# Kernel optimization log

Hardware: AMD Instinct MI355X
Metric: run time of the kernel (lower is better)

## Reference

```python
import jax, jax.numpy as jnp
import numpy as np
import math

B_GRAPHS = 256
L_NODES = 64
N_NODES = B_GRAPHS * L_NODES
N_EDGES = N_NODES * 4
HEADS = 8
D_INNER = 512
N_DAGS = 1
DIAMETER = 64


def setup_inputs() -> dict:
    key = jax.random.key(0)
    ks = jax.random.split(key, 8)
    x = jax.random.normal(ks[0], (N_NODES, D_INNER), jnp.float32)
    B = jax.random.normal(ks[1], (N_NODES, D_INNER), jnp.float32)
    C = jax.random.normal(ks[2], (N_NODES, D_INNER), jnp.float32)
    dt = jax.random.normal(ks[3], (N_NODES, N_DAGS * HEADS * 2), jnp.float32)
    dt_edge = jax.random.normal(ks[4], (N_EDGES, N_DAGS * HEADS), jnp.float32)
    # DAG edges: within each graph, src_local < dst_local (gap 1..7) -> strictly upper triangular
    u = jax.random.randint(ks[5], (N_EDGES,), 0, L_NODES - 1)
    gap = jax.random.randint(ks[6], (N_EDGES,), 1, 8)
    v = jnp.minimum(u + gap, L_NODES - 1)
    graph = jnp.arange(N_EDGES) // (N_EDGES // B_GRAPHS)
    edge_index = jnp.stack([graph * L_NODES + u, graph * L_NODES + v]).astype(jnp.int32)
    data_batch = (jnp.arange(N_NODES) // L_NODES).astype(jnp.int32)
    dag_masks = jnp.ones((N_DAGS, N_EDGES), jnp.float32)
    # dt_bias init as in module __init__ (inverse softplus of dt in [1e-3, 1e-1])
    rng = np.random.default_rng(0)
    dtv = np.exp(rng.uniform(size=(HEADS,)) * (math.log(0.1) - math.log(0.001)) + math.log(0.001))
    dtv = np.clip(dtv, 1e-4, None)
    dt_bias = jnp.asarray(dtv + np.log(-np.expm1(-dtv)), jnp.float32)
    D = jnp.ones((HEADS,), jnp.float32)
    return dict(x=x, B=B, C=C, dt=dt, dt_edge=dt_edge, dt_bias=dt_bias, D=D,
                dag_masks=dag_masks, edge_index=edge_index, data_batch=data_batch,
                diameter=DIAMETER)


def _repeated_squaring_inverse(A, diam):
    # (I - A)^{-1} = prod_k (I + A^{2^k}) for nilpotent A; O(log diam) matmuls
    j = 2 ** int(math.ceil(math.log2(diam)))
    I = jnp.eye(A.shape[-1], dtype=A.dtype)
    last = A
    M = I + A
    for _ in range(2, int(math.log2(j)) + 1):
        last = last @ last
        M = M @ (I + last)
    return M


def reference(x, B, C, dt, dt_edge, dt_bias, D, dag_masks, edge_index, data_batch, diameter):
    N, din = x.shape
    g, E = dag_masks.shape
    n = dt_bias.shape[0]
    b = int(data_batch[-1]) + 1
    l = N // b  # equal-size graphs -> dense batching is a reshape, mask all-True
    h = din // n
    src, dst = edge_index[0], edge_index[1]

    # dt_node: (N, g*n*c) -> (c, g, n, N); softplus(dt + bias)
    c = dt.shape[1] // (g * n)
    dtn = dt.reshape(N, g, n, c).transpose(3, 1, 2, 0)
    dtn = jax.nn.softplus(dtn + dt_bias[None, None, :, None])
    dte = dt_edge.reshape(E, g, n).transpose(1, 2, 0)  # (g,n,E)
    dte = jax.nn.softplus(dte + dt_bias[None, :, None])

    dt_s, dt_t = dtn[0], dtn[1]
    dt_sum = (dt_s[:, :, src] + dt_t[:, :, dst] + dte) / np.sqrt(3.0)  # (g,n,E)
    dt_exp = jnp.exp(-dt_sum)
    msk = dag_masks[:, None, :]
    dt_sum = dt_sum * msk
    dt_exp = dt_exp * msk

    # dense adjacency with per-edge attrs; note 'b l1 l2 (g n) -> b g n l2 l1' transpose
    b_e = src // l
    sl = src % l
    dl = dst % l
    attr = dt_exp.transpose(2, 0, 1).reshape(E, g * n)
    adj = jnp.zeros((b, l, l, g * n), x.dtype).at[b_e, sl, dl].add(attr)
    A = adj.reshape(b, l, l, g, n).transpose(0, 3, 4, 2, 1)  # (b,g,n,l,l)

    # normalize_mat: sqrt outer product of in-degree counts, clamped at 1
    ec = jnp.zeros((g, N), x.dtype).at[:, dst].add(dag_masks)
    ec_dense = ec.T.reshape(b, l, g)
    outer = jnp.sqrt(jnp.einsum('blg,btg->bglt', ec_dense, ec_dense))
    outer = jnp.where(outer < 1.0, 1.0, outer)
    A = A / outer[:, :, None]

    dnorm = jnp.zeros((g, n, N), x.dtype).at[:, :, dst].add(dt_sum)
    dnorm = dnorm.transpose(2, 0, 1).reshape(b, l, g, n).transpose(0, 2, 3, 1)  # (b,g,n,l)

    A2 = A.reshape(b, g * n, l, l).astype(jnp.float32)
    L = _repeated_squaring_inverse(A2, int(diameter))
    L = L.reshape(b, g, n, l, l) * dnorm[..., None]

    x4 = x.reshape(b, l, n, h).transpose(0, 2, 1, 3)  # (b,n,l,h)
    B3 = B.reshape(b, l, -1)
    C3 = C.reshape(b, l, -1)
    # y = einsum(C,L,B,x) with B/C broadcast over (g,n): fold C.B^T into L
    CB = jnp.einsum('bld,btd->blt', C3, B3)
    M = L * CB[:, None, None]
    y = jnp.einsum('bgnlt,bnth->bgnlh', M, x4)
    y = y + x4[:, None] * D[None, None, :, None, None]
    y = y.transpose(0, 3, 1, 2, 4).reshape(N, g, n * h)  # b g n l h -> (N, g, n*h)
    y = y.sum(axis=1) / np.sqrt(g)
    return y
```

## Files before the change

kernel.cpp:

```cpp
#include <hip/hip_runtime.h>
#include <math.h>

#define NGRAPH 256
#define HEADS  8
#define DIN    512
#define EPG    256
#define NEDGE  65536
#define LOG2E 1.44269504088896341f
#define LN2   0.69314718055994531f

typedef short bf16x8 __attribute__((ext_vector_type(8)));
typedef float f32x4 __attribute__((ext_vector_type(4)));

__device__ __forceinline__ float softplusf(float v) {
    if (v > 20.f) return v;
    float t = exp2f(v * LOG2E);
    return LN2 * log2f(1.f + t);
}
__device__ __forceinline__ unsigned short f2bf(float f) {
    union { float f; unsigned u; } c; c.f = f;
    unsigned r = c.u + 0x7fffu + ((c.u >> 16) & 1u);
    return (unsigned short)(r >> 16);
}
__device__ __forceinline__ float bf2f(unsigned short h) {
    union { float f; unsigned u; } c; c.u = ((unsigned)h) << 16;
    return c.f;
}
__device__ __forceinline__ int swz_idx(int row, int t) {
    int g = ((t >> 3) ^ (row ^ (row >> 3))) & 7;
    return (row << 6) | (g << 3) | (t & 7);
}
__device__ __forceinline__ void split1(float f, unsigned short& hi, unsigned short& lo) {
    union { float f; unsigned q; } c; c.f = f;
    unsigned hb = c.q & 0xffff0000u;
    hi = (unsigned short)(hb >> 16);
    union { float f; unsigned q; } d; d.q = hb;
    union { float f; unsigned q; } e2; e2.f = f - d.f;
    lo = (unsigned short)(e2.q >> 16);
}

__device__ __forceinline__ void stage_chunk(int c, unsigned short* buf,
                                            const float* __restrict__ Cm,
                                            const float* __restrict__ Bm,
                                            int b, int tid) {
    #pragma unroll
    for (int i = 0; i < 4; ++i) {
        int u = tid * 4 + i;
        int mat = u >> 10;
        int rem = u & 1023;
        int row = rem >> 4;
        int col4 = (rem & 15) << 2;
        const float* src = (mat ? Bm : Cm) + ((size_t)(b * 64 + row)) * DIN + c * 64 + col4;
        float4 v = *(const float4*)src;
        float a[4] = {v.x, v.y, v.z, v.w};
        unsigned long long hp = 0, lp = 0;
        #pragma unroll
        for (int k = 0; k < 4; ++k) {
            unsigned short h, l;
            split1(a[k], h, l);
            hp |= ((unsigned long long)h) << (16 * k);
            lp |= ((unsigned long long)l) << (16 * k);
        }
        int idx = swz_idx(row, col4);
        unsigned short* thi = buf + (mat ? 8192 : 0);
        *(unsigned long long*)(thi + idx) = hp;
        *(unsigned long long*)(thi + 4096 + idx) = lp;
    }
}

__global__ __launch_bounds__(512, 2) void dag_fused_v3(
        const float* __restrict__ x,
        const float* __restrict__ Bm,
        const float* __restrict__ Cm,
        const float* __restrict__ dt,
        const float* __restrict__ dt_edge,
        const float* __restrict__ dt_bias,
        const float* __restrict__ Dp,
        const float* __restrict__ dag_masks,
        const int* __restrict__ edge_index,
        float* __restrict__ out) {
    __shared__ __align__(16) unsigned short WS[32768];
    __shared__ __align__(16) unsigned short Xt[HEADS][4096];
    __shared__ __align__(16) unsigned short CBsh[4096];
    __shared__ float Ab[HEADS][448];
    __shared__ float dts[HEADS][64];
    __shared__ float dtt[HEADS][64];
    __shared__ float dnsh[HEADS][64];
    __shared__ float ecsh[64];

    const int b = blockIdx.x;
    const int tid = threadIdx.x;
    const int w = tid >> 6;
    const int lane = tid & 63;
    const int lm = lane & 15;
    const int quad = lane >> 4;
    const float bias = dt_bias[w];

    {
        float2 dv = *(const float2*)(dt + ((size_t)(b * 64 + lane)) * 16 + w * 2);
        dts[w][lane] = softplusf(dv.x + bias);
        dtt[w][lane] = softplusf(dv.y + bias);
        dnsh[w][lane] = 0.f;
        #pragma unroll
        for (int s = 0; s < 7; ++s) Ab[w][lane * 7 + s] = 0.f;
        if (w == 0) ecsh[lane] = 0.f;
    }

    {
        #pragma unroll
        for (int eo = 0; eo < 4; ++eo) {
            int e = b * EPG + eo * 64 + lane;
            int sl = edge_index[e] & 63;
            int dl = edge_index[NEDGE + e] & 63;
            float mk = dag_masks[e];
            float de = softplusf(dt_edge[(size_t)e * HEADS + w] + bias);
            float dsum = (dts[w][sl] + dtt[w][dl] + de) * 0.57735026918962576451f;
            float dexp = exp2f(-dsum * LOG2E);
            atomicAdd(&Ab[w][dl * 7 + (dl - sl - 1)], dexp * mk);
            atomicAdd(&dnsh[w][dl], dsum * mk);
            if (w == 0) atomicAdd(&ecsh[dl], mk);
        }
    }

    {
        const float* xg = x + (size_t)b * 64 * DIN + w * 64;
        #pragma unroll
        for (int r = 0; r < 4; ++r) {
            int t0 = quad * 4 + r * 16;
            int e0 = lm * 4;
            float4 v0 = *(const float4*)(xg + (size_t)(t0 + 0) * DIN + e0);
            float4 v1 = *(const float4*)(xg + (size_t)(t0 + 1) * DIN + e0);
            float4 v2 = *(const float4*)(xg + (size_t)(t0 + 2) * DIN + e0);
            float4 v3 = *(const float4*)(xg + (size_t)(t0 + 3) * DIN + e0);
            float a0[4] = {v0.x, v0.y, v0.z, v0.w};
            float a1[4] = {v1.x, v1.y, v1.z, v1.w};
            float a2[4] = {v2.x, v2.y, v2.z, v2.w};
            float a3[4] = {v3.x, v3.y, v3.z, v3.w};
            #pragma unroll
            for (int k = 0; k < 4; ++k) {
                unsigned long long pk =
                      (unsigned long long)f2bf(a0[k])
                    | ((unsigned long long)f2bf(a1[k]) << 16)
                    | ((unsigned long long)f2bf(a2[k]) << 32)
                    | ((unsigned long long)f2bf(a3[k]) << 48);
                *(unsigned long long*)(&Xt[w][swz_idx(e0 + k, t0)]) = pk;
            }
        }
    }

    const int mi = w >> 1;
    const int ni0 = (w & 1) * 2;
    f32x4 acc0 = {0.f, 0.f, 0.f, 0.f};
    f32x4 acc1 = {0.f, 0.f, 0.f, 0.f};
    stage_chunk(0, WS, Cm, Bm, b, tid);
    for (int c = 0; c < 8; ++c) {
        __syncthreads();
        if (c < 7) stage_chunk(c + 1, WS + ((c + 1) & 1) * 16384, Cm, Bm, b, tid);
        const unsigned short* p = WS + (c & 1) * 16384;
        #pragma unroll
        for (int ks = 0; ks < 2; ++ks) {
            int kl = ks * 32 + quad * 8;
            bf16x8 ah  = *(const bf16x8*)(p +         swz_idx(mi * 16 + lm, kl));
            bf16x8 al  = *(const bf16x8*)(p +  4096 + swz_idx(mi * 16 + lm, kl));
            bf16x8 b0h = *(const bf16x8*)(p +  8192 + swz_idx(ni0 * 16 + lm, kl));
            bf16x8 b0l = *(const bf16x8*)(p + 12288 + swz_idx(ni0 * 16 + lm, kl));
            bf16x8 b1h = *(const bf16x8*)(p +  8192 + swz_idx((ni0 + 1) * 16 + lm, kl));
            bf16x8 b1l = *(const bf16x8*)(p + 12288 + swz_idx((ni0 + 1) * 16 + lm, kl));
            acc0 = __builtin_amdgcn_mfma_f32_16x16x32_bf16(ah, b0h, acc0, 0, 0, 0);
            acc0 = __builtin_amdgcn_mfma_f32_16x16x32_bf16(ah, b0l, acc0, 0, 0, 0);
            acc0 = __builtin_amdgcn_mfma_f32_16x16x32_bf16(al, b0h, acc0, 0, 0, 0);
            acc1 = __builtin_amdgcn_mfma_f32_16x16x32_bf16(ah, b1h, acc1, 0, 0, 0);
            acc1 = __builtin_amdgcn_mfma_f32_16x16x32_bf16(ah, b1l, acc1, 0, 0, 0);
            acc1 = __builtin_amdgcn_mfma_f32_16x16x32_bf16(al, b1h, acc1, 0, 0, 0);
        }
    }
    #pragma unroll
    for (int r = 0; r < 4; ++r) {
        int row = mi * 16 + quad * 4 + r;
        CBsh[row * 64 + ni0 * 16 + lm] = f2bf(acc0[r]);
        CBsh[row * 64 + (ni0 + 1) * 16 + lm] = f2bf(acc1[r]);
    }
    __syncthreads();

    {
        float eci = ecsh[lane];
        #pragma unroll
        for (int s = 0; s < 7; ++s) {
            int src = lane - 1 - s;
            if (src >= 0) {
                float p = eci * ecsh[src];
                float f = fminf(1.f, rsqrtf(p));
                Ab[w][lane * 7 + s] *= f;
            }
        }
    }

    unsigned short* Wlw = WS + w * 4096;
    {
        const int j = lane;
        const float Dh = Dp[w];
        float mwin[7] = {0.f, 0.f, 0.f, 0.f, 0.f, 0.f, 0.f};
        float cab[7];
        #pragma unroll
        for (int s = 0; s < 7; ++s) cab[s] = Ab[w][s];
        float cbv = bf2f(CBsh[j]);
        float dnv = dnsh[w][0];
        for (int i = 0; i < 64; ++i) {
            float nab[7], ncb = 0.f, ndn = 0.f;
            if (i < 63) {
                #pragma unroll
                for (int s = 0; s < 7; ++s) nab[s] = Ab[w][(i + 1) * 7 + s];
                ncb = bf2f(CBsh[(i + 1) * 64 + j]);
                ndn = dnsh[w][i + 1];
            } else {
                #pragma unroll
                for (int s = 0; s < 7; ++s) nab[s] = 0.f;
            }
            float diag = (j == i) ? 1.f : 0.f;
            float t0 = fmaf(cab[0], mwin[0], fmaf(cab[1], mwin[1], diag));
            float t1 = fmaf(cab[2], mwin[2], fmaf(cab[3], mwin[3], cab[4] * mwin[4]));
            float t2 = fmaf(cab[5], mwin[5], cab[6] * mwin[6]);
            float mi_ = t0 + (t1 + t2);
            float wv = mi_ * cbv * dnv;
            if (j == i) wv += Dh;
            Wlw[swz_idx(i, j)] = f2bf(wv);
            #pragma unroll
            for (int s = 6; s > 0; --s) mwin[s] = mwin[s - 1];
            mwin[0] = mi_;
            #pragma unroll
            for (int s = 0; s < 7; ++s) cab[s] = nab[s];
            cbv = ncb;
            dnv = ndn;
        }
    }

    {
        bf16x8 bf[4][2];
        #pragma unroll
        for (int eb = 0; eb < 4; ++eb) {
            int er = eb * 16 + lm;
            bf[eb][0] = *(const bf16x8*)(&Xt[w][swz_idx(er, quad * 8)]);
            bf[eb][1] = *(const bf16x8*)(&Xt[w][swz_idx(er, 32 + quad * 8)]);
        }
        float* og = out + (size_t)b * 64 * DIN + w * 64;
        #pragma unroll
        for (int m2 = 0; m2 < 4; ++m2) {
            int row0 = m2 * 16 + lm;
            bf16x8 a0 = *(const bf16x8*)(&Wlw[swz_idx(row0, quad * 8)]);
            bf16x8 a1 = *(const bf16x8*)(&Wlw[swz_idx(row0, 32 + quad * 8)]);
            f32x4 acc[4];
            #pragma unroll
            for (int eb = 0; eb < 4; ++eb) {
                f32x4 z = {0.f, 0.f, 0.f, 0.f};
                z = __builtin_amdgcn_mfma_f32_16x16x32_bf16(a0, bf[eb][0], z, 0, 0, 0);
                z = __builtin_amdgcn_mfma_f32_16x16x32_bf16(a1, bf[eb][1], z, 0, 0, 0);
                acc[eb] = z;
            }
            #pragma unroll
            for (int r = 0; r < 4; ++r) {
                int row = m2 * 16 + quad * 4 + r;
                #pragma unroll
                for (int eb = 0; eb < 4; ++eb)
                    og[(size_t)row * DIN + eb * 16 + lm] = acc[eb][r];
            }
        }
    }
}

extern "C" void kernel_launch(void* const* d_in, const int* in_sizes, int n_in,
                              void* d_out, int out_size, void* d_ws, size_t ws_size,
                              hipStream_t stream) {
    (void)in_sizes; (void)n_in; (void)out_size; (void)d_ws; (void)ws_size;
    dag_fused_v3<<<dim3(NGRAPH), dim3(512), 0, stream>>>(
        (const float*)d_in[0],
        (const float*)d_in[1],
        (const float*)d_in[2],
        (const float*)d_in[3],
        (const float*)d_in[4],
        (const float*)d_in[5],
        (const float*)d_in[6],
        (const float*)d_in[7],
        (const int*)d_in[8],
        (float*)d_out);
}
```

Measured before the change: 163.6 us.

## Split each graph across two blocks by head halves, redundantly computing C·B^T

```diff
diff --git a/kernel.cpp b/kernel.cpp
--- a/kernel.cpp
+++ b/kernel.cpp
@@ -30,6 +30,10 @@
     int g = ((t >> 3) ^ (row ^ (row >> 3))) & 7;
     return (row << 6) | (g << 3) | (t & 7);
 }
+__device__ __forceinline__ int swz32(int row, int t) {
+    int g = ((t >> 3) ^ (row & 3) ^ ((row >> 2) & 3)) & 3;
+    return row * 32 + g * 8 + (t & 7);
+}
 __device__ __forceinline__ void split1(float f, unsigned short& hi, unsigned short& lo) {
     union { float f; unsigned q; } c; c.f = f;
     unsigned hb = c.q & 0xffff0000u;
@@ -39,18 +43,16 @@
     lo = (unsigned short)(e2.q >> 16);
 }
 
-__device__ __forceinline__ void stage_chunk(int c, unsigned short* buf,
-                                            const float* __restrict__ Cm,
-                                            const float* __restrict__ Bm,
-                                            int b, int tid) {
+__device__ __forceinline__ void stage32(int c, unsigned short* buf,
+                                        const float* __restrict__ Cm,
+                                        const float* __restrict__ Bm,
+                                        int b, int tid) {
     #pragma unroll
     for (int i = 0; i < 4; ++i) {
-        int u = tid * 4 + i;
-        int mat = u >> 10;
-        int rem = u & 1023;
-        int row = rem >> 4;
-        int col4 = (rem & 15) << 2;
-        const float* src = (mat ? Bm : Cm) + ((size_t)(b * 64 + row)) * DIN + c * 64 + col4;
+        int rem = ((i & 1) << 8) + tid;
+        int row = rem >> 3;
+        int col4 = (rem & 7) << 2;
+        const float* src = ((i >> 1) ? Bm : Cm) + ((size_t)(b * 64 + row)) * DIN + c * 32 + col4;
         float4 v = *(const float4*)src;
         float a[4] = {v.x, v.y, v.z, v.w};
         unsigned long long hp = 0, lp = 0;
@@ -61,14 +63,14 @@
             hp |= ((unsigned long long)h) << (16 * k);
             lp |= ((unsigned long long)l) << (16 * k);
         }
-        int idx = swz_idx(row, col4);
-        unsigned short* thi = buf + (mat ? 8192 : 0);
-        *(unsigned long long*)(thi + idx) = hp;
-        *(unsigned long long*)(thi + 4096 + idx) = lp;
-    }
-}
-
-__global__ __launch_bounds__(512, 2) void dag_fused_v3(
+        int idx = swz32(row, col4);
+        unsigned short* t2 = buf + (i >> 1) * 4096;
+        *(unsigned long long*)(t2 + idx) = hp;
+        *(unsigned long long*)(t2 + 2048 + idx) = lp;
+    }
+}
+
+__global__ __launch_bounds__(256, 3) void dag_split_v4(
         const float* __restrict__ x,
         const float* __restrict__ Bm,
         const float* __restrict__ Cm,
@@ -79,31 +81,34 @@
         const float* __restrict__ dag_masks,
         const int* __restrict__ edge_index,
         float* __restrict__ out) {
-    __shared__ __align__(16) unsigned short WS[32768];
-    __shared__ __align__(16) unsigned short Xt[HEADS][4096];
+    __shared__ __align__(16) unsigned short WS[16384];
     __shared__ __align__(16) unsigned short CBsh[4096];
-    __shared__ float Ab[HEADS][448];
-    __shared__ float dts[HEADS][64];
-    __shared__ float dtt[HEADS][64];
-    __shared__ float dnsh[HEADS][64];
-    __shared__ float ecsh[64];
-
-    const int b = blockIdx.x;
+    __shared__ __align__(16) float Ab8[4][512];
+    __shared__ float dts[4][64];
+    __shared__ float dtt[4][64];
+    __shared__ float dnsh[4][64];
+    __shared__ float ecsh[4][64];
+
+    const int gid = blockIdx.x;
+    const int b = gid & 255;
+    const int half = gid >> 8;
     const int tid = threadIdx.x;
     const int w = tid >> 6;
     const int lane = tid & 63;
     const int lm = lane & 15;
     const int quad = lane >> 4;
-    const float bias = dt_bias[w];
-
-    {
-        float2 dv = *(const float2*)(dt + ((size_t)(b * 64 + lane)) * 16 + w * 2);
+    const int h = half * 4 + w;
+    const float bias = dt_bias[h];
+
+    {
+        float2 dv = *(const float2*)(dt + ((size_t)(b * 64 + lane)) * 16 + h * 2);
         dts[w][lane] = softplusf(dv.x + bias);
         dtt[w][lane] = softplusf(dv.y + bias);
         dnsh[w][lane] = 0.f;
-        #pragma unroll
-        for (int s = 0; s < 7; ++s) Ab[w][lane * 7 + s] = 0.f;
-        if (w == 0) ecsh[lane] = 0.f;
+        ecsh[w][lane] = 0.f;
+        float4 z = make_float4(0.f, 0.f, 0.f, 0.f);
+        *(float4*)(&Ab8[w][lane * 8]) = z;
+        *(float4*)(&Ab8[w][lane * 8 + 4]) = z;
     }
 
     {
@@ -113,113 +118,86 @@
             int sl = edge_index[e] & 63;
             int dl = edge_index[NEDGE + e] & 63;
             float mk = dag_masks[e];
-            float de = softplusf(dt_edge[(size_t)e * HEADS + w] + bias);
+            float de = softplusf(dt_edge[(size_t)e * HEADS + h] + bias);
             float dsum = (dts[w][sl] + dtt[w][dl] + de) * 0.57735026918962576451f;
             float dexp = exp2f(-dsum * LOG2E);
-            atomicAdd(&Ab[w][dl * 7 + (dl - sl - 1)], dexp * mk);
+            atomicAdd(&Ab8[w][dl * 8 + (dl - sl)], dexp * mk);
             atomicAdd(&dnsh[w][dl], dsum * mk);
-            if (w == 0) atomicAdd(&ecsh[dl], mk);
-        }
-    }
-
-    {
-        const float* xg = x + (size_t)b * 64 * DIN + w * 64;
-        #pragma unroll
-        for (int r = 0; r < 4; ++r) {
-            int t0 = quad * 4 + r * 16;
-            int e0 = lm * 4;
-            float4 v0 = *(const float4*)(xg + (size_t)(t0 + 0) * DIN + e0);
-            float4 v1 = *(const float4*)(xg + (size_t)(t0 + 1) * DIN + e0);
-            float4 v2 = *(const float4*)(xg + (size_t)(t0 + 2) * DIN + e0);
-            float4 v3 = *(const float4*)(xg + (size_t)(t0 + 3) * DIN + e0);
-            float a0[4] = {v0.x, v0.y, v0.z, v0.w};
-            float a1[4] = {v1.x, v1.y, v1.z, v1.w};
-            float a2[4] = {v2.x, v2.y, v2.z, v2.w};
-            float a3[4] = {v3.x, v3.y, v3.z, v3.w};
-            #pragma unroll
-            for (int k = 0; k < 4; ++k) {
-                unsigned long long pk =
-                      (unsigned long long)f2bf(a0[k])
-                    | ((unsigned long long)f2bf(a1[k]) << 16)
-                    | ((unsigned long long)f2bf(a2[k]) << 32)
-                    | ((unsigned long long)f2bf(a3[k]) << 48);
-                *(unsigned long long*)(&Xt[w][swz_idx(e0 + k, t0)]) = pk;
-            }
-        }
-    }
-
-    const int mi = w >> 1;
-    const int ni0 = (w & 1) * 2;
-    f32x4 acc0 = {0.f, 0.f, 0.f, 0.f};
-    f32x4 acc1 = {0.f, 0.f, 0.f, 0.f};
-    stage_chunk(0, WS, Cm, Bm, b, tid);
-    for (int c = 0; c < 8; ++c) {
-        __syncthreads();
-        if (c < 7) stage_chunk(c + 1, WS + ((c + 1) & 1) * 16384, Cm, Bm, b, tid);
-        const unsigned short* p = WS + (c & 1) * 16384;
-        #pragma unroll
-        for (int ks = 0; ks < 2; ++ks) {
-            int kl = ks * 32 + quad * 8;
-            bf16x8 ah  = *(const bf16x8*)(p +         swz_idx(mi * 16 + lm, kl));
-            bf16x8 al  = *(const bf16x8*)(p +  4096 + swz_idx(mi * 16 + lm, kl));
-            bf16x8 b0h = *(const bf16x8*)(p +  8192 + swz_idx(ni0 * 16 + lm, kl));
-            bf16x8 b0l = *(const bf16x8*)(p + 12288 + swz_idx(ni0 * 16 + lm, kl));
-            bf16x8 b1h = *(const bf16x8*)(p +  8192 + swz_idx((ni0 + 1) * 16 + lm, kl));
-            bf16x8 b1l = *(const bf16x8*)(p + 12288 + swz_idx((ni0 + 1) * 16 + lm, kl));
-            acc0 = __builtin_amdgcn_mfma_f32_16x16x32_bf16(ah, b0h, acc0, 0, 0, 0);
-            acc0 = __builtin_amdgcn_mfma_f32_16x16x32_bf16(ah, b0l, acc0, 0, 0, 0);
-            acc0 = __builtin_amdgcn_mfma_f32_16x16x32_bf16(al, b0h, acc0, 0, 0, 0);
-            acc1 = __builtin_amdgcn_mfma_f32_16x16x32_bf16(ah, b1h, acc1, 0, 0, 0);
-            acc1 = __builtin_amdgcn_mfma_f32_16x16x32_bf16(ah, b1l, acc1, 0, 0, 0);
-            acc1 = __builtin_amdgcn_mfma_f32_16x16x32_bf16(al, b1h, acc1, 0, 0, 0);
-        }
-    }
-    #pragma unroll
-    for (int r = 0; r < 4; ++r) {
-        int row = mi * 16 + quad * 4 + r;
-        CBsh[row * 64 + ni0 * 16 + lm] = f2bf(acc0[r]);
-        CBsh[row * 64 + (ni0 + 1) * 16 + lm] = f2bf(acc1[r]);
-    }
-    __syncthreads();
-
-    {
-        float eci = ecsh[lane];
+            atomicAdd(&ecsh[w][dl], mk);
+        }
+    }
+
+    {
+        float eci = ecsh[w][lane];
+        float4 a03 = *(const float4*)(&Ab8[w][lane * 8]);
+        float4 a47 = *(const float4*)(&Ab8[w][lane * 8 + 4]);
+        float sc[7];
         #pragma unroll
         for (int s = 0; s < 7; ++s) {
             int src = lane - 1 - s;
-            if (src >= 0) {
-                float p = eci * ecsh[src];
-                float f = fminf(1.f, rsqrtf(p));
-                Ab[w][lane * 7 + s] *= f;
-            }
-        }
-    }
+            float p = (src >= 0) ? eci * ecsh[w][src] : 1.f;
+            sc[s] = fminf(1.f, rsqrtf(p));
+        }
+        a03.y *= sc[0]; a03.z *= sc[1]; a03.w *= sc[2];
+        a47.x *= sc[3]; a47.y *= sc[4]; a47.z *= sc[5]; a47.w *= sc[6];
+        *(float4*)(&Ab8[w][lane * 8]) = a03;
+        *(float4*)(&Ab8[w][lane * 8 + 4]) = a47;
+    }
+
+    {
+        f32x4 acc[4];
+        #pragma unroll
+        for (int ni = 0; ni < 4; ++ni) acc[ni] = (f32x4){0.f, 0.f, 0.f, 0.f};
+        stage32(0, WS, Cm, Bm, b, tid);
+        for (int c = 0; c < 16; ++c) {
+            __syncthreads();
+            if (c < 15) stage32(c + 1, WS + ((c + 1) & 1) * 8192, Cm, Bm, b, tid);
+            const unsigned short* p = WS + (c & 1) * 8192;
+            bf16x8 ah = *(const bf16x8*)(p + swz32(w * 16 + lm, quad * 8));
+            bf16x8 al = *(const bf16x8*)(p + 2048 + swz32(w * 16 + lm, quad * 8));
+            #pragma unroll
+            for (int ni = 0; ni < 4; ++ni) {
+                bf16x8 bh = *(const bf16x8*)(p + 4096 + swz32(ni * 16 + lm, quad * 8));
+                bf16x8 bl = *(const bf16x8*)(p + 6144 + swz32(ni * 16 + lm, quad * 8));
+                acc[ni] = __builtin_amdgcn_mfma_f32_16x16x32_bf16(ah, bh, acc[ni], 0, 0, 0);
+                acc[ni] = __builtin_amdgcn_mfma_f32_16x16x32_bf16(ah, bl, acc[ni], 0, 0, 0);
+                acc[ni] = __builtin_amdgcn_mfma_f32_16x16x32_bf16(al, bh, acc[ni], 0, 0, 0);
+            }
+        }
+        #pragma unroll
+        for (int ni = 0; ni < 4; ++ni)
+            #pragma unroll
+            for (int r = 0; r < 4; ++r)
+                CBsh[(w * 16 + quad * 4 + r) * 64 + ni * 16 + lm] = f2bf(acc[ni][r]);
+    }
+    __syncthreads();
 
     unsigned short* Wlw = WS + w * 4096;
     {
         const int j = lane;
-        const float Dh = Dp[w];
+        const float Dh = Dp[h];
         float mwin[7] = {0.f, 0.f, 0.f, 0.f, 0.f, 0.f, 0.f};
-        float cab[7];
-        #pragma unroll
-        for (int s = 0; s < 7; ++s) cab[s] = Ab[w][s];
+        float4 a03 = *(const float4*)(&Ab8[w][0]);
+        float4 a47 = *(const float4*)(&Ab8[w][4]);
         float cbv = bf2f(CBsh[j]);
         float dnv = dnsh[w][0];
+        #pragma unroll 2
         for (int i = 0; i < 64; ++i) {
-            float nab[7], ncb = 0.f, ndn = 0.f;
+            float4 n03, n47;
+            float ncb = 0.f, ndn = 0.f;
             if (i < 63) {
-                #pragma unroll
-                for (int s = 0; s < 7; ++s) nab[s] = Ab[w][(i + 1) * 7 + s];
+                n03 = *(const float4*)(&Ab8[w][(i + 1) * 8]);
+                n47 = *(const float4*)(&Ab8[w][(i + 1) * 8 + 4]);
                 ncb = bf2f(CBsh[(i + 1) * 64 + j]);
                 ndn = dnsh[w][i + 1];
             } else {
-                #pragma unroll
-                for (int s = 0; s < 7; ++s) nab[s] = 0.f;
+                n03 = make_float4(0.f, 0.f, 0.f, 0.f);
+                n47 = n03;
             }
             float diag = (j == i) ? 1.f : 0.f;
-            float t0 = fmaf(cab[0], mwin[0], fmaf(cab[1], mwin[1], diag));
-            float t1 = fmaf(cab[2], mwin[2], fmaf(cab[3], mwin[3], cab[4] * mwin[4]));
-            float t2 = fmaf(cab[5], mwin[5], cab[6] * mwin[6]);
+            float t0 = fmaf(a03.y, mwin[0], fmaf(a03.z, mwin[1], diag));
+            float t1 = fmaf(a03.w, mwin[2], fmaf(a47.x, mwin[3], a47.y * mwin[4]));
+            float t2 = fmaf(a47.z, mwin[5], a47.w * mwin[6]);
             float mi_ = t0 + (t1 + t2);
             float wv = mi_ * cbv * dnv;
             if (j == i) wv += Dh;
@@ -227,22 +205,27 @@
             #pragma unroll
             for (int s = 6; s > 0; --s) mwin[s] = mwin[s - 1];
             mwin[0] = mi_;
-            #pragma unroll
-            for (int s = 0; s < 7; ++s) cab[s] = nab[s];
-            cbv = ncb;
-            dnv = ndn;
-        }
-    }
-
-    {
-        bf16x8 bf[4][2];
-        #pragma unroll
-        for (int eb = 0; eb < 4; ++eb) {
-            int er = eb * 16 + lm;
-            bf[eb][0] = *(const bf16x8*)(&Xt[w][swz_idx(er, quad * 8)]);
-            bf[eb][1] = *(const bf16x8*)(&Xt[w][swz_idx(er, 32 + quad * 8)]);
-        }
-        float* og = out + (size_t)b * 64 * DIN + w * 64;
+            a03 = n03; a47 = n47;
+            cbv = ncb; dnv = ndn;
+        }
+    }
+
+    {
+        const float* xh = x + ((size_t)b * 64) * DIN + h * 64;
+        bf16x8 bfr[4][2];
+        #pragma unroll
+        for (int eb = 0; eb < 4; ++eb)
+            #pragma unroll
+            for (int ks = 0; ks < 2; ++ks) {
+                bf16x8 f;
+                #pragma unroll
+                for (int jj = 0; jj < 8; ++jj) {
+                    float xv = xh[(size_t)(ks * 32 + quad * 8 + jj) * DIN + eb * 16 + lm];
+                    f[jj] = (short)f2bf(xv);
+                }
+                bfr[eb][ks] = f;
+            }
+        float* og = out + ((size_t)b * 64) * DIN + h * 64;
         #pragma unroll
         for (int m2 = 0; m2 < 4; ++m2) {
             int row0 = m2 * 16 + lm;
@@ -252,8 +235,8 @@
             #pragma unroll
             for (int eb = 0; eb < 4; ++eb) {
                 f32x4 z = {0.f, 0.f, 0.f, 0.f};
-                z = __builtin_amdgcn_mfma_f32_16x16x32_bf16(a0, bf[eb][0], z, 0, 0, 0);
-                z = __builtin_amdgcn_mfma_f32_16x16x32_bf16(a1, bf[eb][1], z, 0, 0, 0);
+                z = __builtin_amdgcn_mfma_f32_16x16x32_bf16(a0, bfr[eb][0], z, 0, 0, 0);
+                z = __builtin_amdgcn_mfma_f32_16x16x32_bf16(a1, bfr[eb][1], z, 0, 0, 0);
                 acc[eb] = z;
             }
             #pragma unroll
@@ -271,7 +254,7 @@
                               void* d_out, int out_size, void* d_ws, size_t ws_size,
                               hipStream_t stream) {
     (void)in_sizes; (void)n_in; (void)out_size; (void)d_ws; (void)ws_size;
-    dag_fused_v3<<<dim3(NGRAPH), dim3(512), 0, stream>>>(
+    dag_split_v4<<<dim3(512), dim3(256), 0, stream>>>(
         (const float*)d_in[0],
         (const float*)d_in[1],
         (const float*)d_in[2],
```

Measured after the change: 174.6 us. 1.07x slower.
